# Kernel optimization log

Hardware: AMD Instinct MI355X
Metric: run time of the kernel (lower is better)

The kernel has to match this reference:

```python
import jax, jax.numpy as jnp
import numpy as np

N_NODES = 50000
N_EDGES = 800000
NODE_IN = 16
NODE_OUT = 3
H = 128
N_LAYERS = 3


def setup_inputs() -> dict:
    key = jax.random.key(0)
    ks = jax.random.split(key, 16)
    s = 0.05
    inp = {
        "x": jax.random.normal(ks[0], (N_NODES, NODE_IN), dtype=jnp.float32),
        "edge_index": jax.random.randint(ks[1], (2, N_EDGES), 0, N_NODES, dtype=jnp.int64),
        # encoder / decoder
        "enc_w": jax.random.normal(ks[2], (NODE_IN, H), dtype=jnp.float32) * s,
        "enc_b": jnp.zeros((H,), dtype=jnp.float32),
        "dec_w": jax.random.normal(ks[3], (H, NODE_OUT), dtype=jnp.float32) * s,
        "dec_b": jnp.zeros((NODE_OUT,), dtype=jnp.float32),
        # 3 processor layers, edge MLP: Linear(2H,H) -> ReLU -> Linear(H,H)
        "edge_w1": jax.random.normal(ks[4], (N_LAYERS, 2 * H, H), dtype=jnp.float32) * s,
        "edge_b1": jnp.zeros((N_LAYERS, H), dtype=jnp.float32),
        "edge_w2": jax.random.normal(ks[5], (N_LAYERS, H, H), dtype=jnp.float32) * s,
        "edge_b2": jnp.zeros((N_LAYERS, H), dtype=jnp.float32),
        # node MLP: Linear(2H,H) -> ReLU -> Linear(H,H)
        "node_w1": jax.random.normal(ks[6], (N_LAYERS, 2 * H, H), dtype=jnp.float32) * s,
        "node_b1": jnp.zeros((N_LAYERS, H), dtype=jnp.float32),
        "node_w2": jax.random.normal(ks[7], (N_LAYERS, H, H), dtype=jnp.float32) * s,
        "node_b2": jnp.zeros((N_LAYERS, H), dtype=jnp.float32),
    }
    return inp


def reference(x, edge_index, enc_w, enc_b, dec_w, dec_b,
              edge_w1, edge_b1, edge_w2, edge_b2,
              node_w1, node_b1, node_w2, node_b2):
    row = edge_index[0]  # source nodes
    col = edge_index[1]  # destination nodes
    h = x @ enc_w + enc_b  # [N, H]
    for l in range(N_LAYERS):
        # EdgeModel: cat(src, dest) -> MLP
        e_in = jnp.concatenate([h[row], h[col]], axis=1)  # [E, 2H]
        e = jnp.maximum(e_in @ edge_w1[l] + edge_b1[l], 0.0) @ edge_w2[l] + edge_b2[l]  # [E, H]
        # NodeModel: scatter_add messages by col, cat with x -> MLP
        agg = jax.ops.segment_sum(e, col, num_segments=h.shape[0])  # [N, H]
        n_in = jnp.concatenate([h, agg], axis=1)  # [N, 2H]
        h_upd = jnp.maximum(n_in @ node_w1[l] + node_b1[l], 0.0) @ node_w2[l] + node_b2[l]
        h = h + h_upd  # residual
    return h @ dec_w + dec_b  # [N, NODE_OUT]
```

## Files before the change

### kernel.cpp

```cpp
#include <hip/hip_runtime.h>
#include <hip/hip_bf16.h>
#include <stdint.h>

#define N_NODES 50000
#define N_EDGES 800000
#define HID 128
#define NODE_IN 16
#define NODE_OUT 3
#define NODE_TILES 782
#define SCAN_BLOCKS 196
#define EDGE_BLOCKS 3125
#define MFOLD_BLOCKS 192
#define DGB 16
#define EDBLOCKS 3125

typedef __attribute__((ext_vector_type(8))) short short8;
typedef __attribute__((ext_vector_type(4))) float f32x4;
typedef __attribute__((ext_vector_type(4))) unsigned int u32x4;

__device__ __forceinline__ unsigned short f2bf(float f) {
    union { float f; unsigned int u; } v; v.f = f;
    unsigned int u = v.u;
    u += 0x7fff + ((u >> 16) & 1);
    return (unsigned short)(u >> 16);
}
__device__ __forceinline__ float bf2f(unsigned short s) {
    union { unsigned int u; float f; } v; v.u = ((unsigned int)s) << 16;
    return v.f;
}
__device__ __forceinline__ float bfu_lo(unsigned int u) {
    union { unsigned int u; float f; } v; v.u = u << 16; return v.f;
}
__device__ __forceinline__ float bfu_hi(unsigned int u) {
    union { unsigned int u; float f; } v; v.u = u & 0xffff0000u; return v.f;
}
__device__ __forceinline__ unsigned int cvt_pk_bf16(float lo, float hi) {
    unsigned int r;
    asm("v_cvt_pk_bf16_f32 %0, %1, %2" : "=v"(r) : "v"(lo), "v"(hi));
    return r;
}

__global__ __launch_bounds__(256) void k1_fused(
    const int* __restrict__ colp, int* __restrict__ cnt, int* __restrict__ rank,
    const float* __restrict__ edge_w2, const float* __restrict__ node_w1,
    const float* __restrict__ edge_b2,
    float* __restrict__ Mtmp, float* __restrict__ Vtmp,
    const float* __restrict__ x, const float* __restrict__ enc_w,
    const float* __restrict__ enc_b, unsigned short* __restrict__ h) {
    __shared__ float wts[NODE_IN * HID];
    __shared__ float bts[HID];
    __shared__ float xs[64][NODE_IN];
    int b = blockIdx.x, t = threadIdx.x;
    if (b < EDGE_BLOCKS) {
        int e = b * 256 + t;
        rank[e] = atomicAdd(&cnt[colp[e]], 1);
    } else if (b < EDGE_BLOCKS + MFOLD_BLOCKS) {
        int d = (b - EDGE_BLOCKS) * 256 + t;
        int L = d / 16384, rem = d & 16383;
        int k = rem >> 7, n = rem & 127;
        const float* w2  = edge_w2 + (size_t)L * 16384;
        const float* w1b = node_w1 + (size_t)L * 32768 + 16384;
        float acc = 0.f;
        #pragma unroll 4
        for (int j = 0; j < 128; j++) acc += w2[k * 128 + j] * w1b[j * 128 + n];
        Mtmp[d] = acc;
        if (k == 0) {
            const float* b2 = edge_b2 + (size_t)L * 128;
            float vv = 0.f;
            #pragma unroll 4
            for (int j = 0; j < 128; j++) vv += b2[j] * w1b[j * 128 + n];
            Vtmp[L * 128 + n] = vv;
        }
    } else {
        int b2 = b - EDGE_BLOCKS - MFOLD_BLOCKS;
        int n0 = b2 * 64;
        for (int i = t; i < NODE_IN * HID; i += 256) wts[i] = enc_w[i];
        if (t < HID) bts[t] = enc_b[t];
        for (int i = t; i < 64 * NODE_IN; i += 256) {
            int nl = i >> 4, ii = i & 15;
            int n = n0 + nl;
            xs[nl][ii] = (n < N_NODES) ? x[n * NODE_IN + ii] : 0.f;
        }
        __syncthreads();
        for (int o = t; o < 64 * HID; o += 256) {
            int nl = o >> 7, cc = o & 127;
            float acc = bts[cc];
            #pragma unroll
            for (int i = 0; i < NODE_IN; i++) acc += xs[nl][i] * wts[i * HID + cc];
            int n = n0 + nl;
            if (n < N_NODES) h[n * HID + cc] = f2bf(acc);
        }
    }
}

__global__ __launch_bounds__(256) void k2a_scan1_swizzle(
    const int* __restrict__ cnt, int* __restrict__ ex, int* __restrict__ bsums,
    const float* __restrict__ edge_w1, const float* __restrict__ node_w1,
    const float* __restrict__ node_w2, const float* __restrict__ Mtmp,
    unsigned short* __restrict__ swz) {
    __shared__ int s[256];
    int b = blockIdx.x, t = threadIdx.x;
    if (b < SCAN_BLOCKS) {
        int i = b * 256 + t;
        int v = (i < N_NODES) ? cnt[i] : 0;
        s[t] = v;
        __syncthreads();
        for (int off = 1; off < 256; off <<= 1) {
            int u = (t >= off) ? s[t - off] : 0;
            __syncthreads();
            s[t] += u;
            __syncthreads();
        }
        if (i < N_NODES) ex[i] = s[t] - v;
        if (t == 255) bsums[b] = s[255];
    } else {
        for (int d = (b - SCAN_BLOCKS) * 256 + t; d < 3 * 98304;
             d += (gridDim.x - SCAN_BLOCKS) * 256) {
            int L = d / 98304;
            int rem = d - L * 98304;
            unsigned short* base = swz + L * 98304;
            if (rem < 32768) {
                const float* w1 = edge_w1 + (size_t)L * 32768;
                int j = rem & 7, ll = (rem >> 3) & 63, tt = rem >> 9;
                int nt = tt & 15, kt = tt >> 4;
                int k = kt * 32 + ((ll >> 4) << 3) + j;
                int cc = nt * 16 + (ll & 15);
                float v = (cc < 128) ? w1[k * 128 + cc] : w1[(128 + k) * 128 + (cc - 128)];
                base[rem] = f2bf(v);
            } else if (rem < 49152) {
            } else if (rem < 81920) {
                int d2 = rem - 49152;
                int j = d2 & 7, ll = (d2 >> 3) & 63, tt = d2 >> 9;
                int nt = tt & 7, kt = tt >> 3;
                int k = kt * 32 + ((ll >> 4) << 3) + j, n = (nt << 4) + (ll & 15);
                float v = (k < 128) ? node_w1[(size_t)L * 32768 + k * 128 + n]
                                    : Mtmp[(size_t)L * 16384 + (k - 128) * 128 + n];
                base[rem] = f2bf(v);
            } else {
                int d2 = rem - 81920;
                const float* src = node_w2 + (size_t)L * 16384;
                int j = d2 & 7, ll = (d2 >> 3) & 63, tt = d2 >> 9;
                int nt = tt & 7, kt = tt >> 3;
                int k = kt * 32 + ((ll >> 4) << 3) + j, n = (nt << 4) + (ll & 15);
                base[rem] = f2bf(src[k * 128 + n]);
            }
        }
    }
}

__global__ __launch_bounds__(256) void k3_scatter_sd(
    const int* __restrict__ rowp, const int* __restrict__ colp,
    const int* __restrict__ ex, const int* __restrict__ bsums,
    const int* __restrict__ rank, int* __restrict__ rsrt, int* __restrict__ ex2,
    const unsigned short* __restrict__ h, const unsigned short* __restrict__ w1c,
    const float* __restrict__ eb1,
    unsigned short* __restrict__ S, unsigned short* __restrict__ D) {
    __shared__ int sc[256];
    __shared__ int ls[SCAN_BLOCKS];
    __shared__ unsigned short hs[64][136];
    int b = blockIdx.x, t = threadIdx.x;
    if (b < EDGE_BLOCKS) {
        int v = (t < SCAN_BLOCKS) ? bsums[t] : 0;
        sc[t] = v;
        __syncthreads();
        for (int off = 1; off < 256; off <<= 1) {
            int u = (t >= off) ? sc[t - off] : 0;
            __syncthreads();
            sc[t] += u;
            __syncthreads();
        }
        if (t < SCAN_BLOCKS) ls[t] = sc[t] - v;
        __syncthreads();

        if (b < SCAN_BLOCKS) {
            int i = b * 256 + t;
            if (i < N_NODES) ex2[i] = ex[i] + ls[b];
        }
        int e = b * 256 + t;
        int c = colp[e];
        int pos = ex[c] + ls[c >> 8] + rank[e];
        rsrt[pos] = rowp[e];
    } else {
        int b2 = b - EDGE_BLOCKS;
        int wave = t >> 6, l = t & 63, q = l >> 4, l16 = l & 15;
        int nt0s = wave * 4;
        int n0 = b2 * 64;
        for (int i = t; i < 64 * 16; i += 256) {
            int nl = i >> 4, li = i & 15;
            int n = n0 + nl;
            short8 v = (short8){0, 0, 0, 0, 0, 0, 0, 0};
            if (n < N_NODES) v = *(const short8*)(h + (size_t)n * HID + li * 8);
            *(short8*)&hs[nl][li * 8] = v;
        }
        short8 wr[4][4];
        #pragma unroll
        for (int kt = 0; kt < 4; kt++)
            #pragma unroll
            for (int i = 0; i < 4; i++)
                wr[kt][i] = *(const short8*)(w1c + ((kt * 16 + nt0s + i) * 64 + l) * 8);
        __syncthreads();

        f32x4 acc[4][4];
        #pragma unroll
        for (int g = 0; g < 4; g++)
            #pragma unroll
            for (int i = 0; i < 4; i++) acc[g][i] = (f32x4){0.f, 0.f, 0.f, 0.f};
        #pragma unroll
        for (int kt = 0; kt < 4; kt++) {
            #pragma unroll
            for (int g = 0; g < 4; g++) {
                short8 a = *(const short8*)&hs[g * 16 + l16][kt * 32 + q * 8];
                #pragma unroll
                for (int i = 0; i < 4; i++)
                    acc[g][i] = __builtin_amdgcn_mfma_f32_16x16x32_bf16(a, wr[kt][i], acc[g][i], 0, 0, 0);
            }
        }
        #pragma unroll
        for (int i = 0; i < 4; i++) {
            int cc = (nt0s + i) * 16 + l16;
            float badd = 0.f;
            if (cc >= 128) badd = eb1[cc - 128];
            #pragma unroll
            for (int g = 0; g < 4; g++)
                #pragma unroll
                for (int r = 0; r < 4; r++) {
                    int n = n0 + g * 16 + q * 4 + r;
                    if (n < N_NODES) {
                        unsigned short v = f2bf(acc[g][i][r] + badd);
                        if (cc < 128) S[n * HID + cc] = v;
                        else          D[n * HID + (cc - 128)] = v;
                    }
                }
        }
    }
}

__global__ __launch_bounds__(256, 8) void edge_kernel(
    const unsigned short* __restrict__ S, const unsigned short* __restrict__ D,
    const int* __restrict__ rsrt, const int* __restrict__ ex2,
    float* __restrict__ aggH)
{
    int t = threadIdx.x;
    int g16 = t >> 4, ch = t & 15;

    const int q = EDBLOCKS / 8, r = EDBLOCKS % 8;
    int xcd = blockIdx.x & 7, slot = blockIdx.x >> 3;
    int cntx = q + (xcd < r);
    if (slot >= cntx) return;
    int myb = xcd * q + (xcd < r ? xcd : r) + slot;

    int d = myb * DGB + g16;
    int e0 = ex2[d];
    int e1 = (d < N_NODES - 1) ? ex2[d + 1] : N_EDGES;

    short8 dv = *(const short8*)(D + (size_t)d * HID + ch * 8);
    float dr[8];
    #pragma unroll
    for (int p = 0; p < 4; p++) {
        unsigned int ud = ((const unsigned int*)&dv)[p];
        dr[2 * p]     = bfu_lo(ud);
        dr[2 * p + 1] = bfu_hi(ud);
    }

    float a[8];
    #pragma unroll
    for (int j = 0; j < 8; j++) a[j] = 0.f;

    auto ldS = [&](int e) -> short8 {
        int rn = rsrt[e];
        return *(const short8*)(S + (size_t)rn * HID + ch * 8);
    };
    auto accum = [&](const short8& sv) {
        #pragma unroll
        for (int p = 0; p < 4; p++) {
            unsigned int us = ((const unsigned int*)&sv)[p];
            float v0 = bfu_lo(us) + dr[2 * p];
            float v1 = bfu_hi(us) + dr[2 * p + 1];
            v0 = v0 > 0.f ? v0 : 0.f;
            v1 = v1 > 0.f ? v1 : 0.f;
            a[2 * p]     += v0;
            a[2 * p + 1] += v1;
        }
    };

    int e = e0;
    short8 s0 = (short8){0, 0, 0, 0, 0, 0, 0, 0};
    short8 s1 = s0;
    if (e < e1)     s0 = ldS(e);
    if (e + 1 < e1) s1 = ldS(e + 1);
    for (; e + 2 < e1; e += 2) {
        short8 n0v = ldS(e + 2);
        short8 n1v = (e + 3 < e1) ? ldS(e + 3) : (short8){0, 0, 0, 0, 0, 0, 0, 0};
        accum(s0);
        accum(s1);
        s0 = n0v;
        s1 = n1v;
    }
    if (e < e1)     accum(s0);
    if (e + 1 < e1) accum(s1);

    f32x4* dst = (f32x4*)(aggH + (size_t)d * HID + ch * 8);
    dst[0] = (f32x4){a[0], a[1], a[2], a[3]};
    dst[1] = (f32x4){a[4], a[5], a[6], a[7]};
}

template<int LAST>
__global__ __launch_bounds__(256, 4) void node_kernel(
    unsigned short* __restrict__ h, float* __restrict__ aggH, const int* __restrict__ cnt,
    const unsigned short* __restrict__ w1m_s, const float* __restrict__ b1,
    const float* __restrict__ vfold,
    const unsigned short* __restrict__ w2s, const float* __restrict__ b2,
    const unsigned short* __restrict__ w1c_next, const float* __restrict__ eb1n,
    unsigned short* __restrict__ S, unsigned short* __restrict__ D,
    const float* __restrict__ dec_w, const float* __restrict__ dec_b, float* __restrict__ out)
{
    __shared__ unsigned short in_h[64][136];
    __shared__ unsigned short in_a[64][136];
    __shared__ int cnt_s[64];
    __shared__ float dw[HID * NODE_OUT];
    __shared__ float db[NODE_OUT];
    int t = threadIdx.x, wave = t >> 6, l = t & 63, q = l >> 4, l16 = l & 15;
    int nt0 = wave * 2, nt0s = wave * 4;
    int n0 = blockIdx.x * 64;

    if (LAST) {
        for (int i = t; i < HID * NODE_OUT; i += 256) dw[i] = dec_w[i];
        if (t < NODE_OUT) db[t] = dec_b[t];
    }

    #pragma unroll
    for (int it = 0; it < 8; it++) {
        int g = it * 256 + t;
        int nl = g >> 5, sub = g & 31, half = sub >> 4, li = sub & 15;
        int n = n0 + nl;
        short8 v = (short8){0, 0, 0, 0, 0, 0, 0, 0};
        if (n < N_NODES) {
            if (half == 0) {
                v = *(const short8*)(h + n * HID + li * 8);
            } else {
                const float* ap = aggH + n * HID + li * 8;
                f32x4 a0 = *(const f32x4*)ap, a1 = *(const f32x4*)(ap + 4);
                unsigned int* vp = (unsigned int*)&v;
                vp[0] = cvt_pk_bf16(a0[0], a0[1]);
                vp[1] = cvt_pk_bf16(a0[2], a0[3]);
                vp[2] = cvt_pk_bf16(a1[0], a1[1]);
                vp[3] = cvt_pk_bf16(a1[2], a1[3]);
            }
        }
        if (half == 0) *(short8*)&in_h[nl][li * 8] = v;
        else           *(short8*)&in_a[nl][li * 8] = v;
    }
    if (t < 64) cnt_s[t] = (n0 + t < N_NODES) ? cnt[n0 + t] : 0;
    __syncthreads();

    float b1r0 = b1[nt0 * 16 + l16], b1r1 = b1[(nt0 + 1) * 16 + l16];
    float vr0 = vfold[nt0 * 16 + l16], vr1 = vfold[(nt0 + 1) * 16 + l16];
    float b2r0 = b2[nt0 * 16 + l16], b2r1 = b2[(nt0 + 1) * 16 + l16];

    f32x4 acc[4][2];
    #pragma unroll
    for (int g = 0; g < 4; g++)
        #pragma unroll
        for (int j = 0; j < 2; j++) acc[g][j] = (f32x4){0.f, 0.f, 0.f, 0.f};
    #pragma unroll
    for (int kt = 0; kt < 8; kt++) {
        short8 b0 = *(const short8*)(w1m_s + ((kt * 8 + nt0)     * 64 + l) * 8);
        short8 b1v = *(const short8*)(w1m_s + ((kt * 8 + nt0 + 1) * 64 + l) * 8);
        #pragma unroll
        for (int g = 0; g < 4; g++) {
            short8 a = (kt < 4) ? *(const short8*)&in_h[g * 16 + l16][kt * 32 + q * 8]
                                : *(const short8*)&in_a[g * 16 + l16][(kt - 4) * 32 + q * 8];
            acc[g][0] = __builtin_amdgcn_mfma_f32_16x16x32_bf16(a, b0, acc[g][0], 0, 0, 0);
            acc[g][1] = __builtin_amdgcn_mfma_f32_16x16x32_bf16(a, b1v, acc[g][1], 0, 0, 0);
        }
    }
    __syncthreads();

    #pragma unroll
    for (int j = 0; j < 2; j++) {
        float bv = j ? b1r1 : b1r0;
        float vv = j ? vr1 : vr0;
        #pragma unroll
        for (int g = 0; g < 4; g++)
            #pragma unroll
            for (int r = 0; r < 4; r++) {
                int m2 = g * 16 + q * 4 + r;
                float v = acc[g][j][r] + bv + (float)cnt_s[m2] * vv;
                v = v > 0.f ? v : 0.f;
                in_a[m2][(nt0 + j) * 16 + l16] = f2bf(v);
            }
    }
    __syncthreads();

    f32x4 acc2[4][2];
    #pragma unroll
    for (int g = 0; g < 4; g++)
        #pragma unroll
        for (int j = 0; j < 2; j++) acc2[g][j] = (f32x4){0.f, 0.f, 0.f, 0.f};
    #pragma unroll
    for (int kt = 0; kt < 4; kt++) {
        short8 b0 = *(const short8*)(w2s + ((kt * 8 + nt0)     * 64 + l) * 8);
        short8 b1v = *(const short8*)(w2s + ((kt * 8 + nt0 + 1) * 64 + l) * 8);
        #pragma unroll
        for (int g = 0; g < 4; g++) {
            short8 a = *(const short8*)&in_a[g * 16 + l16][kt * 32 + q * 8];
            acc2[g][0] = __builtin_amdgcn_mfma_f32_16x16x32_bf16(a, b0, acc2[g][0], 0, 0, 0);
            acc2[g][1] = __builtin_amdgcn_mfma_f32_16x16x32_bf16(a, b1v, acc2[g][1], 0, 0, 0);
        }
    }
    #pragma unroll
    for (int j = 0; j < 2; j++) {
        float bv = j ? b2r1 : b2r0;
        #pragma unroll
        for (int g = 0; g < 4; g++)
            #pragma unroll
            for (int r = 0; r < 4; r++) {
                float v = acc2[g][j][r] + bv;
                int m2 = g * 16 + q * 4 + r;
                int n = n0 + m2;
                if (n < N_NODES) {
                    int c = (nt0 + j) * 16 + l16;
                    unsigned short nh = f2bf(bf2f(in_h[m2][c]) + v);
                    if (!LAST) h[n * HID + c] = nh;
                    in_h[m2][c] = nh;
                }
            }
    }
    __syncthreads();

    if (!LAST) {
        #pragma unroll
        for (int p = 0; p < 2; p++) {
            short8 wr[4][2];
            #pragma unroll
            for (int kt = 0; kt < 4; kt++) {
                wr[kt][0] = *(const short8*)(w1c_next + ((kt * 16 + nt0s + p * 2)     * 64 + l) * 8);
                wr[kt][1] = *(const short8*)(w1c_next + ((kt * 16 + nt0s + p * 2 + 1) * 64 + l) * 8);
            }
            f32x4 accs[4][2];
            #pragma unroll
            for (int g = 0; g < 4; g++)
                #pragma unroll
                for (int i = 0; i < 2; i++) accs[g][i] = (f32x4){0.f, 0.f, 0.f, 0.f};
            #pragma unroll
            for (int kt = 0; kt < 4; kt++) {
                #pragma unroll
                for (int g = 0; g < 4; g++) {
                    short8 a = *(const short8*)&in_h[g * 16 + l16][kt * 32 + q * 8];
                    accs[g][0] = __builtin_amdgcn_mfma_f32_16x16x32_bf16(a, wr[kt][0], accs[g][0], 0, 0, 0);
                    accs[g][1] = __builtin_amdgcn_mfma_f32_16x16x32_bf16(a, wr[kt][1], accs[g][1], 0, 0, 0);
                }
            }
            #pragma unroll
            for (int i = 0; i < 2; i++) {
                int c = (nt0s + p * 2 + i) * 16 + l16;
                float badd = 0.f;
                if (c >= 128) badd = eb1n[c - 128];
                #pragma unroll
                for (int g = 0; g < 4; g++)
                    #pragma unroll
                    for (int r = 0; r < 4; r++) {
                        int n = n0 + g * 16 + q * 4 + r;
                        if (n < N_NODES) {
                            unsigned short v = f2bf(accs[g][i][r] + badd);
                            if (c < 128) S[n * HID + c] = v;
                            else         D[n * HID + (c - 128)] = v;
                        }
                    }
            }
        }
    } else {
        if (t < 64 * NODE_OUT) {
            int nl = t / 3, o = t - 3 * nl;
            int n = n0 + nl;
            if (n < N_NODES) {
                float a = db[o];
                #pragma unroll 4
                for (int k = 0; k < HID; k++) a += bf2f(in_h[nl][k]) * dw[k * 3 + o];
                out[n * 3 + o] = a;
            }
        }
    }
}

extern "C" void kernel_launch(void* const* d_in, const int* in_sizes, int n_in,
                              void* d_out, int out_size, void* d_ws, size_t ws_size,
                              hipStream_t stream) {
    const float* x       = (const float*)d_in[0];
    const int*   ei      = (const int*)d_in[1];
    const float* enc_w   = (const float*)d_in[2];
    const float* enc_b   = (const float*)d_in[3];
    const float* dec_w   = (const float*)d_in[4];
    const float* dec_b   = (const float*)d_in[5];
    const float* edge_w1 = (const float*)d_in[6];
    const float* edge_b1 = (const float*)d_in[7];
    const float* edge_w2 = (const float*)d_in[8];
    const float* edge_b2 = (const float*)d_in[9];
    const float* node_w1 = (const float*)d_in[10];
    const float* node_b1 = (const float*)d_in[11];
    const float* node_w2 = (const float*)d_in[12];
    const float* node_b2 = (const float*)d_in[13];

    char* ws = (char*)d_ws;
    unsigned short* h    = (unsigned short*)ws;
    float*          aggH = (float*)(ws + 12800000);
    unsigned short* swz  = (unsigned short*)(ws + 38400000);
    int* cnt             = (int*)(ws + 38989824);
    int* ex              = (int*)(ws + 39189824);
    int* bsums           = (int*)(ws + 39389824);
    int* rsrt            = (int*)(ws + 39390848);
    unsigned short* Sbuf = (unsigned short*)(ws + 45790848);
    unsigned short* Dbuf = (unsigned short*)(ws + 58590848);
    float* Mtmp          = (float*)(ws + 71390848);
    float* Vtmp          = (float*)(ws + 71587456);
    int* ex2             = (int*)(ws + 71588992);
    int* rank            = (int*)(ws + 72000000);

    const int* rowp = ei;
    const int* colp = ei + N_EDGES;

    hipMemsetAsync(cnt, 0, (size_t)N_NODES * 4, stream);

    k1_fused<<<EDGE_BLOCKS + MFOLD_BLOCKS + NODE_TILES, 256, 0, stream>>>(
        colp, cnt, rank, edge_w2, node_w1, edge_b2, Mtmp, Vtmp,
        x, enc_w, enc_b, h);
    k2a_scan1_swizzle<<<SCAN_BLOCKS + 288, 256, 0, stream>>>(cnt, ex, bsums, edge_w1,
                                                             node_w1, node_w2, Mtmp, swz);
    k3_scatter_sd<<<EDGE_BLOCKS + NODE_TILES, 256, 0, stream>>>(
        rowp, colp, ex, bsums, rank, rsrt, ex2,
        h, swz , edge_b1 , Sbuf, Dbuf);

    for (int L = 0; L < 3; L++) {
        unsigned short* base = swz + (size_t)L * 98304;
        unsigned short* next = swz + (size_t)(L + 1) * 98304;
        edge_kernel<<<3128, 256, 0, stream>>>(Sbuf, Dbuf, rsrt, ex2, aggH);
        if (L < 2) {
            node_kernel<0><<<NODE_TILES, 256, 0, stream>>>(
                h, aggH, cnt,
                base + 49152, node_b1 + (size_t)L * HID, Vtmp + (size_t)L * HID,
                base + 81920, node_b2 + (size_t)L * HID,
                next, edge_b1 + (size_t)(L + 1) * HID, Sbuf, Dbuf, dec_w, dec_b, (float*)d_out);
        } else {
            node_kernel<1><<<NODE_TILES, 256, 0, stream>>>(
                h, aggH, cnt,
                base + 49152, node_b1 + (size_t)L * HID, Vtmp + (size_t)L * HID,
                base + 81920, node_b2 + (size_t)L * HID,
                base , edge_b1 , Sbuf, Dbuf, dec_w, dec_b, (float*)d_out);
        }
    }
}
```

Before: 364.9 us.

## Fuse edge aggregation into node kernel with double-buffered S/D/h

Merges the per-layer edge gather-aggregate kernel into the node MLP kernel. Each 512-thread block now gathers the incoming messages for its 64 destination nodes straight into shared memory as bf16, so the fp32 aggH round trip through global memory and one launch per layer go away. S, D and h are double-buffered so the next layer's projections don't overwrite rows other blocks are still reading. The weight swizzle work is also redistributed between k1 and k2a. The trade-off is fewer, larger blocks doing irregular gathers, plus lost XCD-aware block mapping, which may reduce latency hiding.

```diff
diff --git a/kernel.cpp b/kernel.cpp
--- a/kernel.cpp
+++ b/kernel.cpp
@@ -11,8 +11,8 @@
 #define SCAN_BLOCKS 196
 #define EDGE_BLOCKS 3125
 #define MFOLD_BLOCKS 192
-#define DGB 16
-#define EDBLOCKS 3125
+#define SWZA_BLOCKS 576
+#define SWZB_BLOCKS 384
 
 typedef __attribute__((ext_vector_type(8))) short short8;
 typedef __attribute__((ext_vector_type(4))) float f32x4;
@@ -46,7 +46,9 @@
     const float* __restrict__ edge_b2,
     float* __restrict__ Mtmp, float* __restrict__ Vtmp,
     const float* __restrict__ x, const float* __restrict__ enc_w,
-    const float* __restrict__ enc_b, unsigned short* __restrict__ h) {
+    const float* __restrict__ enc_b, unsigned short* __restrict__ h,
+    const float* __restrict__ edge_w1, const float* __restrict__ node_w2,
+    unsigned short* __restrict__ swz) {
     __shared__ float wts[NODE_IN * HID];
     __shared__ float bts[HID];
     __shared__ float xs[64][NODE_IN];
@@ -71,7 +73,7 @@
             for (int j = 0; j < 128; j++) vv += b2[j] * w1b[j * 128 + n];
             Vtmp[L * 128 + n] = vv;
         }
-    } else {
+    } else if (b < EDGE_BLOCKS + MFOLD_BLOCKS + NODE_TILES) {
         int b2 = b - EDGE_BLOCKS - MFOLD_BLOCKS;
         int n0 = b2 * 64;
         for (int i = t; i < NODE_IN * HID; i += 256) wts[i] = enc_w[i];
@@ -90,13 +92,32 @@
             int n = n0 + nl;
             if (n < N_NODES) h[n * HID + cc] = f2bf(acc);
         }
+    } else {
+        int d = (b - EDGE_BLOCKS - MFOLD_BLOCKS - NODE_TILES) * 256 + t;
+        int L = d / 49152, rem2 = d - L * 49152;
+        unsigned short* base = swz + L * 98304;
+        if (rem2 < 32768) {
+            const float* w1 = edge_w1 + (size_t)L * 32768;
+            int j = rem2 & 7, ll = (rem2 >> 3) & 63, tt = rem2 >> 9;
+            int nt = tt & 15, kt = tt >> 4;
+            int k = kt * 32 + ((ll >> 4) << 3) + j;
+            int cc = nt * 16 + (ll & 15);
+            float v = (cc < 128) ? w1[k * 128 + cc] : w1[(128 + k) * 128 + (cc - 128)];
+            base[rem2] = f2bf(v);
+        } else {
+            int d2 = rem2 - 32768;
+            const float* src = node_w2 + (size_t)L * 16384;
+            int j = d2 & 7, ll = (d2 >> 3) & 63, tt = d2 >> 9;
+            int nt = tt & 7, kt = tt >> 3;
+            int k = kt * 32 + ((ll >> 4) << 3) + j, n = (nt << 4) + (ll & 15);
+            base[81920 + d2] = f2bf(src[k * 128 + n]);
+        }
     }
 }
 
 __global__ __launch_bounds__(256) void k2a_scan1_swizzle(
     const int* __restrict__ cnt, int* __restrict__ ex, int* __restrict__ bsums,
-    const float* __restrict__ edge_w1, const float* __restrict__ node_w1,
-    const float* __restrict__ node_w2, const float* __restrict__ Mtmp,
+    const float* __restrict__ node_w1, const float* __restrict__ Mtmp,
     unsigned short* __restrict__ swz) {
     __shared__ int s[256];
     int b = blockIdx.x, t = threadIdx.x;
@@ -114,37 +135,15 @@
         if (i < N_NODES) ex[i] = s[t] - v;
         if (t == 255) bsums[b] = s[255];
     } else {
-        for (int d = (b - SCAN_BLOCKS) * 256 + t; d < 3 * 98304;
-             d += (gridDim.x - SCAN_BLOCKS) * 256) {
-            int L = d / 98304;
-            int rem = d - L * 98304;
-            unsigned short* base = swz + L * 98304;
-            if (rem < 32768) {
-                const float* w1 = edge_w1 + (size_t)L * 32768;
-                int j = rem & 7, ll = (rem >> 3) & 63, tt = rem >> 9;
-                int nt = tt & 15, kt = tt >> 4;
-                int k = kt * 32 + ((ll >> 4) << 3) + j;
-                int cc = nt * 16 + (ll & 15);
-                float v = (cc < 128) ? w1[k * 128 + cc] : w1[(128 + k) * 128 + (cc - 128)];
-                base[rem] = f2bf(v);
-            } else if (rem < 49152) {
-            } else if (rem < 81920) {
-                int d2 = rem - 49152;
-                int j = d2 & 7, ll = (d2 >> 3) & 63, tt = d2 >> 9;
-                int nt = tt & 7, kt = tt >> 3;
-                int k = kt * 32 + ((ll >> 4) << 3) + j, n = (nt << 4) + (ll & 15);
-                float v = (k < 128) ? node_w1[(size_t)L * 32768 + k * 128 + n]
-                                    : Mtmp[(size_t)L * 16384 + (k - 128) * 128 + n];
-                base[rem] = f2bf(v);
-            } else {
-                int d2 = rem - 81920;
-                const float* src = node_w2 + (size_t)L * 16384;
-                int j = d2 & 7, ll = (d2 >> 3) & 63, tt = d2 >> 9;
-                int nt = tt & 7, kt = tt >> 3;
-                int k = kt * 32 + ((ll >> 4) << 3) + j, n = (nt << 4) + (ll & 15);
-                base[rem] = f2bf(src[k * 128 + n]);
-            }
-        }
+        int d = (b - SCAN_BLOCKS) * 256 + t;
+        int L = d / 32768, d2 = d - L * 32768;
+        unsigned short* base = swz + L * 98304;
+        int j = d2 & 7, ll = (d2 >> 3) & 63, tt = d2 >> 9;
+        int nt = tt & 7, kt = tt >> 3;
+        int k = kt * 32 + ((ll >> 4) << 3) + j, n = (nt << 4) + (ll & 15);
+        float v = (k < 128) ? node_w1[(size_t)L * 32768 + k * 128 + n]
+                            : Mtmp[(size_t)L * 16384 + (k - 128) * 128 + n];
+        base[49152 + d2] = f2bf(v);
     }
 }
 
@@ -235,239 +234,210 @@
     }
 }
 
-__global__ __launch_bounds__(256, 8) void edge_kernel(
+template<int LAST>
+__global__ __launch_bounds__(512, 4) void layer_kernel(
     const unsigned short* __restrict__ S, const unsigned short* __restrict__ D,
     const int* __restrict__ rsrt, const int* __restrict__ ex2,
-    float* __restrict__ aggH)
-{
-    int t = threadIdx.x;
-    int g16 = t >> 4, ch = t & 15;
-
-    const int q = EDBLOCKS / 8, r = EDBLOCKS % 8;
-    int xcd = blockIdx.x & 7, slot = blockIdx.x >> 3;
-    int cntx = q + (xcd < r);
-    if (slot >= cntx) return;
-    int myb = xcd * q + (xcd < r ? xcd : r) + slot;
-
-    int d = myb * DGB + g16;
-    int e0 = ex2[d];
-    int e1 = (d < N_NODES - 1) ? ex2[d + 1] : N_EDGES;
-
-    short8 dv = *(const short8*)(D + (size_t)d * HID + ch * 8);
-    float dr[8];
-    #pragma unroll
-    for (int p = 0; p < 4; p++) {
-        unsigned int ud = ((const unsigned int*)&dv)[p];
-        dr[2 * p]     = bfu_lo(ud);
-        dr[2 * p + 1] = bfu_hi(ud);
-    }
-
-    float a[8];
-    #pragma unroll
-    for (int j = 0; j < 8; j++) a[j] = 0.f;
-
-    auto ldS = [&](int e) -> short8 {
-        int rn = rsrt[e];
-        return *(const short8*)(S + (size_t)rn * HID + ch * 8);
-    };
-    auto accum = [&](const short8& sv) {
-        #pragma unroll
-        for (int p = 0; p < 4; p++) {
-            unsigned int us = ((const unsigned int*)&sv)[p];
-            float v0 = bfu_lo(us) + dr[2 * p];
-            float v1 = bfu_hi(us) + dr[2 * p + 1];
-            v0 = v0 > 0.f ? v0 : 0.f;
-            v1 = v1 > 0.f ? v1 : 0.f;
-            a[2 * p]     += v0;
-            a[2 * p + 1] += v1;
-        }
-    };
-
-    int e = e0;
-    short8 s0 = (short8){0, 0, 0, 0, 0, 0, 0, 0};
-    short8 s1 = s0;
-    if (e < e1)     s0 = ldS(e);
-    if (e + 1 < e1) s1 = ldS(e + 1);
-    for (; e + 2 < e1; e += 2) {
-        short8 n0v = ldS(e + 2);
-        short8 n1v = (e + 3 < e1) ? ldS(e + 3) : (short8){0, 0, 0, 0, 0, 0, 0, 0};
-        accum(s0);
-        accum(s1);
-        s0 = n0v;
-        s1 = n1v;
-    }
-    if (e < e1)     accum(s0);
-    if (e + 1 < e1) accum(s1);
-
-    f32x4* dst = (f32x4*)(aggH + (size_t)d * HID + ch * 8);
-    dst[0] = (f32x4){a[0], a[1], a[2], a[3]};
-    dst[1] = (f32x4){a[4], a[5], a[6], a[7]};
-}
-
-template<int LAST>
-__global__ __launch_bounds__(256, 4) void node_kernel(
-    unsigned short* __restrict__ h, float* __restrict__ aggH, const int* __restrict__ cnt,
+    const unsigned short* __restrict__ h, unsigned short* __restrict__ hn,
     const unsigned short* __restrict__ w1m_s, const float* __restrict__ b1,
     const float* __restrict__ vfold,
     const unsigned short* __restrict__ w2s, const float* __restrict__ b2,
     const unsigned short* __restrict__ w1c_next, const float* __restrict__ eb1n,
-    unsigned short* __restrict__ S, unsigned short* __restrict__ D,
-    const float* __restrict__ dec_w, const float* __restrict__ dec_b, float* __restrict__ out)
+    unsigned short* __restrict__ Sn, unsigned short* __restrict__ Dn,
+    const float* __restrict__ dec_w, const float* __restrict__ dec_b,
+    float* __restrict__ out)
 {
     __shared__ unsigned short in_h[64][136];
     __shared__ unsigned short in_a[64][136];
-    __shared__ int cnt_s[64];
+    __shared__ int deg_s[64];
     __shared__ float dw[HID * NODE_OUT];
     __shared__ float db[NODE_OUT];
-    int t = threadIdx.x, wave = t >> 6, l = t & 63, q = l >> 4, l16 = l & 15;
-    int nt0 = wave * 2, nt0s = wave * 4;
+    int t = threadIdx.x;
     int n0 = blockIdx.x * 64;
 
-    if (LAST) {
-        for (int i = t; i < HID * NODE_OUT; i += 256) dw[i] = dec_w[i];
-        if (t < NODE_OUT) db[t] = dec_b[t];
-    }
-
-    #pragma unroll
-    for (int it = 0; it < 8; it++) {
-        int g = it * 256 + t;
-        int nl = g >> 5, sub = g & 31, half = sub >> 4, li = sub & 15;
+    #pragma unroll
+    for (int i = t; i < 64 * 16; i += 512) {
+        int nl = i >> 4, li = i & 15;
         int n = n0 + nl;
         short8 v = (short8){0, 0, 0, 0, 0, 0, 0, 0};
-        if (n < N_NODES) {
-            if (half == 0) {
-                v = *(const short8*)(h + n * HID + li * 8);
-            } else {
-                const float* ap = aggH + n * HID + li * 8;
-                f32x4 a0 = *(const f32x4*)ap, a1 = *(const f32x4*)(ap + 4);
-                unsigned int* vp = (unsigned int*)&v;
-                vp[0] = cvt_pk_bf16(a0[0], a0[1]);
-                vp[1] = cvt_pk_bf16(a0[2], a0[3]);
-                vp[2] = cvt_pk_bf16(a1[0], a1[1]);
-                vp[3] = cvt_pk_bf16(a1[2], a1[3]);
+        if (n < N_NODES) v = *(const short8*)(h + (size_t)n * HID + li * 8);
+        *(short8*)&in_h[nl][li * 8] = v;
+    }
+    if (LAST) {
+        if (t < HID * NODE_OUT) dw[t] = dec_w[t];
+        if (t < NODE_OUT) db[t] = dec_b[t];
+    }
+
+    {
+        int g8 = t >> 3, ch8 = t & 7;
+        int d = n0 + g8;
+        float a[16];
+        #pragma unroll
+        for (int j = 0; j < 16; j++) a[j] = 0.f;
+
+        if (d < N_NODES) {
+            int e0 = ex2[d];
+            int e1 = (d == N_NODES - 1) ? N_EDGES : ex2[d + 1];
+            if (ch8 == 0) deg_s[g8] = e1 - e0;
+
+            const unsigned short* drow = D + (size_t)d * HID + ch8 * 16;
+            short8 dva = *(const short8*)drow;
+            short8 dvb = *(const short8*)(drow + 8);
+            float dr[16];
+            #pragma unroll
+            for (int p = 0; p < 4; p++) {
+                unsigned int ua = ((const unsigned int*)&dva)[p];
+                unsigned int ub = ((const unsigned int*)&dvb)[p];
+                dr[2 * p]         = bfu_lo(ua);
+                dr[2 * p + 1]     = bfu_hi(ua);
+                dr[8 + 2 * p]     = bfu_lo(ub);
+                dr[8 + 2 * p + 1] = bfu_hi(ub);
             }
-        }
-        if (half == 0) *(short8*)&in_h[nl][li * 8] = v;
-        else           *(short8*)&in_a[nl][li * 8] = v;
-    }
-    if (t < 64) cnt_s[t] = (n0 + t < N_NODES) ? cnt[n0 + t] : 0;
+
+            auto ldS = [&](int e, short8& va, short8& vb) {
+                int rn = rsrt[e];
+                const unsigned short* p = S + (size_t)rn * HID + ch8 * 16;
+                va = *(const short8*)p;
+                vb = *(const short8*)(p + 8);
+            };
+            auto accum = [&](const short8& va, const short8& vb) {
+                #pragma unroll
+                for (int p = 0; p < 4; p++) {
+                    unsigned int ua = ((const unsigned int*)&va)[p];
+                    float v0 = bfu_lo(ua) + dr[2 * p];
+                    float v1 = bfu_hi(ua) + dr[2 * p + 1];
+                    a[2 * p]     += v0 > 0.f ? v0 : 0.f;
+                    a[2 * p + 1] += v1 > 0.f ? v1 : 0.f;
+                    unsigned int ub = ((const unsigned int*)&vb)[p];
+                    float w0 = bfu_lo(ub) + dr[8 + 2 * p];
+                    float w1 = bfu_hi(ub) + dr[8 + 2 * p + 1];
+                    a[8 + 2 * p]     += w0 > 0.f ? w0 : 0.f;
+                    a[8 + 2 * p + 1] += w1 > 0.f ? w1 : 0.f;
+                }
+            };
+
+            int e = e0;
+            short8 s0a = (short8){0,0,0,0,0,0,0,0}, s0b = s0a, s1a = s0a, s1b = s0a;
+            if (e < e1)     ldS(e, s0a, s0b);
+            if (e + 1 < e1) ldS(e + 1, s1a, s1b);
+            for (; e + 2 < e1; e += 2) {
+                short8 p0a, p0b, p1a, p1b;
+                ldS(e + 2, p0a, p0b);
+                if (e + 3 < e1) ldS(e + 3, p1a, p1b);
+                else { p1a = (short8){0,0,0,0,0,0,0,0}; p1b = p1a; }
+                accum(s0a, s0b);
+                accum(s1a, s1b);
+                s0a = p0a; s0b = p0b; s1a = p1a; s1b = p1b;
+            }
+            if (e < e1)     accum(s0a, s0b);
+            if (e + 1 < e1) accum(s1a, s1b);
+        } else if (ch8 == 0) {
+            deg_s[g8] = 0;
+        }
+
+        u32x4 oa, ob;
+        #pragma unroll
+        for (int p = 0; p < 4; p++) {
+            oa[p] = cvt_pk_bf16(a[2 * p], a[2 * p + 1]);
+            ob[p] = cvt_pk_bf16(a[8 + 2 * p], a[8 + 2 * p + 1]);
+        }
+        *(u32x4*)&in_a[g8][ch8 * 16]     = oa;
+        *(u32x4*)&in_a[g8][ch8 * 16 + 8] = ob;
+    }
     __syncthreads();
 
-    float b1r0 = b1[nt0 * 16 + l16], b1r1 = b1[(nt0 + 1) * 16 + l16];
-    float vr0 = vfold[nt0 * 16 + l16], vr1 = vfold[(nt0 + 1) * 16 + l16];
-    float b2r0 = b2[nt0 * 16 + l16], b2r1 = b2[(nt0 + 1) * 16 + l16];
-
-    f32x4 acc[4][2];
+    int wave = t >> 6, l = t & 63, q = l >> 4, l16 = l & 15;
+    int nt = wave;
+    float b1r = b1[nt * 16 + l16];
+    float vr  = vfold[nt * 16 + l16];
+    float b2r = b2[nt * 16 + l16];
+
+    f32x4 acc[4];
+    #pragma unroll
+    for (int g = 0; g < 4; g++) acc[g] = (f32x4){0.f, 0.f, 0.f, 0.f};
+    #pragma unroll
+    for (int kt = 0; kt < 8; kt++) {
+        short8 bfr = *(const short8*)(w1m_s + ((kt * 8 + nt) * 64 + l) * 8);
+        #pragma unroll
+        for (int g = 0; g < 4; g++) {
+            short8 afr = (kt < 4) ? *(const short8*)&in_h[g * 16 + l16][kt * 32 + q * 8]
+                                  : *(const short8*)&in_a[g * 16 + l16][(kt - 4) * 32 + q * 8];
+            acc[g] = __builtin_amdgcn_mfma_f32_16x16x32_bf16(afr, bfr, acc[g], 0, 0, 0);
+        }
+    }
+    __syncthreads();
+
     #pragma unroll
     for (int g = 0; g < 4; g++)
         #pragma unroll
-        for (int j = 0; j < 2; j++) acc[g][j] = (f32x4){0.f, 0.f, 0.f, 0.f};
-    #pragma unroll
-    for (int kt = 0; kt < 8; kt++) {
-        short8 b0 = *(const short8*)(w1m_s + ((kt * 8 + nt0)     * 64 + l) * 8);
-        short8 b1v = *(const short8*)(w1m_s + ((kt * 8 + nt0 + 1) * 64 + l) * 8);
+        for (int r = 0; r < 4; r++) {
+            int m2 = g * 16 + q * 4 + r;
+            float v = acc[g][r] + b1r + (float)deg_s[m2] * vr;
+            v = v > 0.f ? v : 0.f;
+            in_a[m2][nt * 16 + l16] = f2bf(v);
+        }
+    __syncthreads();
+
+    f32x4 acc2[4];
+    #pragma unroll
+    for (int g = 0; g < 4; g++) acc2[g] = (f32x4){0.f, 0.f, 0.f, 0.f};
+    #pragma unroll
+    for (int kt = 0; kt < 4; kt++) {
+        short8 bfr = *(const short8*)(w2s + ((kt * 8 + nt) * 64 + l) * 8);
         #pragma unroll
         for (int g = 0; g < 4; g++) {
-            short8 a = (kt < 4) ? *(const short8*)&in_h[g * 16 + l16][kt * 32 + q * 8]
-                                : *(const short8*)&in_a[g * 16 + l16][(kt - 4) * 32 + q * 8];
-            acc[g][0] = __builtin_amdgcn_mfma_f32_16x16x32_bf16(a, b0, acc[g][0], 0, 0, 0);
-            acc[g][1] = __builtin_amdgcn_mfma_f32_16x16x32_bf16(a, b1v, acc[g][1], 0, 0, 0);
-        }
-    }
+            short8 afr = *(const short8*)&in_a[g * 16 + l16][kt * 32 + q * 8];
+            acc2[g] = __builtin_amdgcn_mfma_f32_16x16x32_bf16(afr, bfr, acc2[g], 0, 0, 0);
+        }
+    }
+    #pragma unroll
+    for (int g = 0; g < 4; g++)
+        #pragma unroll
+        for (int r = 0; r < 4; r++) {
+            int m2 = g * 16 + q * 4 + r;
+            int n = n0 + m2;
+            if (n < N_NODES) {
+                int c = nt * 16 + l16;
+                unsigned short nh = f2bf(bf2f(in_h[m2][c]) + acc2[g][r] + b2r);
+                if (!LAST) hn[n * HID + c] = nh;
+                in_h[m2][c] = nh;
+            }
+        }
     __syncthreads();
 
-    #pragma unroll
-    for (int j = 0; j < 2; j++) {
-        float bv = j ? b1r1 : b1r0;
-        float vv = j ? vr1 : vr0;
-        #pragma unroll
-        for (int g = 0; g < 4; g++)
-            #pragma unroll
-            for (int r = 0; r < 4; r++) {
-                int m2 = g * 16 + q * 4 + r;
-                float v = acc[g][j][r] + bv + (float)cnt_s[m2] * vv;
-                v = v > 0.f ? v : 0.f;
-                in_a[m2][(nt0 + j) * 16 + l16] = f2bf(v);
-            }
-    }
-    __syncthreads();
-
-    f32x4 acc2[4][2];
-    #pragma unroll
-    for (int g = 0; g < 4; g++)
-        #pragma unroll
-        for (int j = 0; j < 2; j++) acc2[g][j] = (f32x4){0.f, 0.f, 0.f, 0.f};
-    #pragma unroll
-    for (int kt = 0; kt < 4; kt++) {
-        short8 b0 = *(const short8*)(w2s + ((kt * 8 + nt0)     * 64 + l) * 8);
-        short8 b1v = *(const short8*)(w2s + ((kt * 8 + nt0 + 1) * 64 + l) * 8);
-        #pragma unroll
-        for (int g = 0; g < 4; g++) {
-            short8 a = *(const short8*)&in_a[g * 16 + l16][kt * 32 + q * 8];
-            acc2[g][0] = __builtin_amdgcn_mfma_f32_16x16x32_bf16(a, b0, acc2[g][0], 0, 0, 0);
-            acc2[g][1] = __builtin_amdgcn_mfma_f32_16x16x32_bf16(a, b1v, acc2[g][1], 0, 0, 0);
-        }
-    }
-    #pragma unroll
-    for (int j = 0; j < 2; j++) {
-        float bv = j ? b2r1 : b2r0;
-        #pragma unroll
-        for (int g = 0; g < 4; g++)
-            #pragma unroll
-            for (int r = 0; r < 4; r++) {
-                float v = acc2[g][j][r] + bv;
-                int m2 = g * 16 + q * 4 + r;
-                int n = n0 + m2;
-                if (n < N_NODES) {
-                    int c = (nt0 + j) * 16 + l16;
-                    unsigned short nh = f2bf(bf2f(in_h[m2][c]) + v);
-                    if (!LAST) h[n * HID + c] = nh;
-                    in_h[m2][c] = nh;
-                }
-            }
-    }
-    __syncthreads();
-
     if (!LAST) {
         #pragma unroll
         for (int p = 0; p < 2; p++) {
-            short8 wr[4][2];
-            #pragma unroll
-            for (int kt = 0; kt < 4; kt++) {
-                wr[kt][0] = *(const short8*)(w1c_next + ((kt * 16 + nt0s + p * 2)     * 64 + l) * 8);
-                wr[kt][1] = *(const short8*)(w1c_next + ((kt * 16 + nt0s + p * 2 + 1) * 64 + l) * 8);
-            }
-            f32x4 accs[4][2];
-            #pragma unroll
-            for (int g = 0; g < 4; g++)
-                #pragma unroll
-                for (int i = 0; i < 2; i++) accs[g][i] = (f32x4){0.f, 0.f, 0.f, 0.f};
+            int nt16 = wave * 2 + p;
+            short8 wr[4];
+            #pragma unroll
+            for (int kt = 0; kt < 4; kt++)
+                wr[kt] = *(const short8*)(w1c_next + ((kt * 16 + nt16) * 64 + l) * 8);
+            f32x4 accs[4];
+            #pragma unroll
+            for (int g = 0; g < 4; g++) accs[g] = (f32x4){0.f, 0.f, 0.f, 0.f};
             #pragma unroll
             for (int kt = 0; kt < 4; kt++) {
                 #pragma unroll
                 for (int g = 0; g < 4; g++) {
-                    short8 a = *(const short8*)&in_h[g * 16 + l16][kt * 32 + q * 8];
-                    accs[g][0] = __builtin_amdgcn_mfma_f32_16x16x32_bf16(a, wr[kt][0], accs[g][0], 0, 0, 0);
-                    accs[g][1] = __builtin_amdgcn_mfma_f32_16x16x32_bf16(a, wr[kt][1], accs[g][1], 0, 0, 0);
+                    short8 afr = *(const short8*)&in_h[g * 16 + l16][kt * 32 + q * 8];
+                    accs[g] = __builtin_amdgcn_mfma_f32_16x16x32_bf16(afr, wr[kt], accs[g], 0, 0, 0);
                 }
             }
-            #pragma unroll
-            for (int i = 0; i < 2; i++) {
-                int c = (nt0s + p * 2 + i) * 16 + l16;
-                float badd = 0.f;
-                if (c >= 128) badd = eb1n[c - 128];
+            int c = nt16 * 16 + l16;
+            float badd = 0.f;
+            if (c >= 128) badd = eb1n[c - 128];
+            #pragma unroll
+            for (int g = 0; g < 4; g++)
                 #pragma unroll
-                for (int g = 0; g < 4; g++)
-                    #pragma unroll
-                    for (int r = 0; r < 4; r++) {
-                        int n = n0 + g * 16 + q * 4 + r;
-                        if (n < N_NODES) {
-                            unsigned short v = f2bf(accs[g][i][r] + badd);
-                            if (c < 128) S[n * HID + c] = v;
-                            else         D[n * HID + (c - 128)] = v;
-                        }
+                for (int r = 0; r < 4; r++) {
+                    int n = n0 + g * 16 + q * 4 + r;
+                    if (n < N_NODES) {
+                        unsigned short v = f2bf(accs[g][r] + badd);
+                        if (c < 128) Sn[n * HID + c] = v;
+                        else         Dn[n * HID + (c - 128)] = v;
                     }
-            }
+                }
         }
     } else {
         if (t < 64 * NODE_OUT) {
@@ -502,50 +472,60 @@
     const float* node_b2 = (const float*)d_in[13];
 
     char* ws = (char*)d_ws;
-    unsigned short* h    = (unsigned short*)ws;
-    float*          aggH = (float*)(ws + 12800000);
-    unsigned short* swz  = (unsigned short*)(ws + 38400000);
-    int* cnt             = (int*)(ws + 38989824);
-    int* ex              = (int*)(ws + 39189824);
-    int* bsums           = (int*)(ws + 39389824);
-    int* rsrt            = (int*)(ws + 39390848);
-    unsigned short* Sbuf = (unsigned short*)(ws + 45790848);
-    unsigned short* Dbuf = (unsigned short*)(ws + 58590848);
-    float* Mtmp          = (float*)(ws + 71390848);
-    float* Vtmp          = (float*)(ws + 71587456);
-    int* ex2             = (int*)(ws + 71588992);
-    int* rank            = (int*)(ws + 72000000);
+    unsigned short* h0   = (unsigned short*)ws;
+    unsigned short* h1   = (unsigned short*)(ws + 12800000);
+    unsigned short* swz  = (unsigned short*)(ws + 25600000);
+    int* cnt             = (int*)(ws + 26189824);
+    int* ex              = (int*)(ws + 26389824);
+    int* bsums           = (int*)(ws + 26589824);
+    int* rsrt            = (int*)(ws + 26590848);
+    unsigned short* S0   = (unsigned short*)(ws + 29790848);
+    unsigned short* D0   = (unsigned short*)(ws + 42590848);
+    unsigned short* S1   = (unsigned short*)(ws + 55390848);
+    unsigned short* D1   = (unsigned short*)(ws + 68190848);
+    float* Mtmp          = (float*)(ws + 80990848);
+    float* Vtmp          = (float*)(ws + 81187456);
+    int* ex2             = (int*)(ws + 81188992);
+    int* rank            = (int*)(ws + 81388992);
 
     const int* rowp = ei;
     const int* colp = ei + N_EDGES;
 
     hipMemsetAsync(cnt, 0, (size_t)N_NODES * 4, stream);
 
-    k1_fused<<<EDGE_BLOCKS + MFOLD_BLOCKS + NODE_TILES, 256, 0, stream>>>(
+    k1_fused<<<EDGE_BLOCKS + MFOLD_BLOCKS + NODE_TILES + SWZA_BLOCKS, 256, 0, stream>>>(
         colp, cnt, rank, edge_w2, node_w1, edge_b2, Mtmp, Vtmp,
-        x, enc_w, enc_b, h);
-    k2a_scan1_swizzle<<<SCAN_BLOCKS + 288, 256, 0, stream>>>(cnt, ex, bsums, edge_w1,
-                                                             node_w1, node_w2, Mtmp, swz);
+        x, enc_w, enc_b, h0, edge_w1, node_w2, swz);
+    k2a_scan1_swizzle<<<SCAN_BLOCKS + SWZB_BLOCKS, 256, 0, stream>>>(
+        cnt, ex, bsums, node_w1, Mtmp, swz);
     k3_scatter_sd<<<EDGE_BLOCKS + NODE_TILES, 256, 0, stream>>>(
         rowp, colp, ex, bsums, rank, rsrt, ex2,
-        h, swz , edge_b1 , Sbuf, Dbuf);
-
+        h0, swz , edge_b1 , S0, D0);
+
+    unsigned short* Sc = S0; unsigned short* Dc = D0;
+    unsigned short* Sn = S1; unsigned short* Dn = D1;
+    unsigned short* hc = h0; unsigned short* hx = h1;
     for (int L = 0; L < 3; L++) {
         unsigned short* base = swz + (size_t)L * 98304;
         unsigned short* next = swz + (size_t)(L + 1) * 98304;
-        edge_kernel<<<3128, 256, 0, stream>>>(Sbuf, Dbuf, rsrt, ex2, aggH);
         if (L < 2) {
-            node_kernel<0><<<NODE_TILES, 256, 0, stream>>>(
-                h, aggH, cnt,
+            layer_kernel<0><<<NODE_TILES, 512, 0, stream>>>(
+                Sc, Dc, rsrt, ex2, hc, hx,
                 base + 49152, node_b1 + (size_t)L * HID, Vtmp + (size_t)L * HID,
                 base + 81920, node_b2 + (size_t)L * HID,
-                next, edge_b1 + (size_t)(L + 1) * HID, Sbuf, Dbuf, dec_w, dec_b, (float*)d_out);
+                next, edge_b1 + (size_t)(L + 1) * HID, Sn, Dn,
+                dec_w, dec_b, (float*)d_out);
+            { unsigned short* tp;
+              tp = Sc; Sc = Sn; Sn = tp;
+              tp = Dc; Dc = Dn; Dn = tp;
+              tp = hc; hc = hx; hx = tp; }
         } else {
-            node_kernel<1><<<NODE_TILES, 256, 0, stream>>>(
-                h, aggH, cnt,
+            layer_kernel<1><<<NODE_TILES, 512, 0, stream>>>(
+                Sc, Dc, rsrt, ex2, hc, hx ,
                 base + 49152, node_b1 + (size_t)L * HID, Vtmp + (size_t)L * HID,
                 base + 81920, node_b2 + (size_t)L * HID,
-                base , edge_b1 , Sbuf, Dbuf, dec_w, dec_b, (float*)d_out);
-        }
-    }
-}
+                base , edge_b1 , Sn , Dn ,
+                dec_w, dec_b, (float*)d_out);
+        }
+    }
+}
```

Measured after the change: 364.6 us. About the same (-0.1%).
